# Optimization experiments

Hardware: AMD Instinct MI355X
Metric: run time of the kernel (lower is better)

The kernel has to match this reference:

```python
import jax, jax.numpy as jnp
import numpy as np

B, S, E, H = 8, 1024, 768, 12
D = E // H  # per-head dim


def setup_inputs() -> dict:
    key = jax.random.key(0)
    ks = jax.random.split(key, 9)
    glorot = lambda k: jax.random.normal(k, (E, E), jnp.float32) * np.sqrt(2.0 / (E + E))
    return {
        "inputs": jax.random.normal(ks[0], (B, S, E), jnp.float32),
        "Wq": glorot(ks[1]), "bq": jnp.zeros((E,), jnp.float32),
        "Wk": glorot(ks[2]), "bk": jnp.zeros((E,), jnp.float32),
        "Wv": glorot(ks[3]), "bv": jnp.zeros((E,), jnp.float32),
        "Wo": glorot(ks[4]), "bo": jnp.zeros((E,), jnp.float32),
    }


def reference(inputs, Wq, bq, Wk, bk, Wv, bv, Wo, bo):
    b, s, e = inputs.shape
    # QKV projections then split heads: [B,S,E] -> [B,H,S,D]
    def heads(x):
        return x.reshape(b, s, H, D).transpose(0, 2, 1, 3)
    q = heads(inputs @ Wq + bq)
    k = heads(inputs @ Wk + bk)
    v = heads(inputs @ Wv + bv)
    scale = 1.0 / jnp.sqrt(jnp.asarray(D, inputs.dtype))
    scores = jnp.einsum("bhqd,bhkd->bhqk", q, k) * scale
    weights = jax.nn.softmax(scores, axis=-1)  # attn_drop rate 0 -> identity
    attn = jnp.einsum("bhqk,bhkd->bhqd", weights, v)
    concat = attn.transpose(0, 2, 1, 3).reshape(b, s, e)
    out = concat @ Wo + bo  # proj_drop rate 0 -> identity
    return out
```

## Files before the change

### kernel.cpp

```cpp
#include <hip/hip_runtime.h>
#include <math.h>

#define BB 8
#define SS 1024
#define EE 768
#define HH 12
#define DD 64
#define MM (BB*SS)

typedef __attribute__((ext_vector_type(8))) short short8;
typedef __attribute__((ext_vector_type(4))) short short4v;
typedef __attribute__((ext_vector_type(4))) float f32x4;
typedef __attribute__((ext_vector_type(4))) int int4v;

static __device__ __forceinline__ short f2bf(float x) {
    unsigned u = __float_as_uint(x);
    u += 0x7fffu + ((u >> 16) & 1u);
    return (short)(u >> 16);
}
static __device__ __forceinline__ int cvtpk_bf16(float lo, float hi) {
    int r;
    asm("v_cvt_pk_bf16_f32 %0, %1, %2" : "=v"(r) : "v"(lo), "v"(hi));
    return r;
}
static __device__ __forceinline__ short8 i4_to_s8(int4v v) {
    union { int4v i; short8 s; } u; u.i = v; return u.s;
}

static __device__ __forceinline__ void gload_lds16(const void* g, void* l) {
    __builtin_amdgcn_global_load_lds((__attribute__((address_space(1))) void*)g,
                                     (__attribute__((address_space(3))) void*)l,
                                     16, 0, 0);
}

#define BAR __builtin_amdgcn_s_barrier()
#define VMW(n) asm volatile("s_waitcnt vmcnt(" #n ")" ::: "memory")

__global__ __launch_bounds__(256)
void prep(const float* __restrict__ X, short* __restrict__ Xb,
          const float* __restrict__ W0, const float* __restrict__ W1,
          const float* __restrict__ W2, const float* __restrict__ W3,
          short* __restrict__ Wt) {
    const int tid = threadIdx.x;
    if (blockIdx.x < 6144) {
        const long i = ((long)blockIdx.x * 256 + tid) * 4;
        float4 v = *(const float4*)&X[i];
        short4v o;
        o.x = f2bf(v.x); o.y = f2bf(v.y); o.z = f2bf(v.z); o.w = f2bf(v.w);
        *(short4v*)&Xb[i] = o;
        return;
    }
    __shared__ short T[64][72];
    const int id = blockIdx.x - 6144;
    const int z  = id / 144;
    const int r2 = id % 144;
    const int i0 = (r2 / 12) * 64;
    const int j0 = (r2 % 12) * 64;
    const float* sp = (z == 0) ? W0 : (z == 1) ? W1 : (z == 2) ? W2 : W3;
    short* dp = Wt + (long)z * EE * EE;
#pragma unroll
    for (int rep = 0; rep < 4; ++rep) {
        const int r = (tid >> 4) + rep * 16;
        const int c = (tid & 15) * 4;
        float4 v = *(const float4*)&sp[(long)(i0 + r) * EE + j0 + c];
        T[c + 0][r] = f2bf(v.x);
        T[c + 1][r] = f2bf(v.y);
        T[c + 2][r] = f2bf(v.z);
        T[c + 3][r] = f2bf(v.w);
    }
    __syncthreads();
#pragma unroll
    for (int rep = 0; rep < 4; ++rep) {
        const int rr = (tid >> 4) + rep * 16;
        const int cc = (tid & 15) * 4;
        short4v o;
        o.x = T[rr][cc + 0]; o.y = T[rr][cc + 1];
        o.z = T[rr][cc + 2]; o.w = T[rr][cc + 3];
        *(short4v*)&dp[(long)(j0 + rr) * EE + i0 + cc] = o;
    }
}

#define GEMM_CORE(Abase, Bbase, row0, col0)                                     \
    f32x4 acc[4][4];                                                            \
    _Pragma("unroll") for (int i = 0; i < 4; ++i)                               \
        _Pragma("unroll") for (int j = 0; j < 4; ++j)                           \
            acc[i][j] = (f32x4){0.f, 0.f, 0.f, 0.f};                            \
    const int rm = (w & 1) * 64, cn = (w >> 1) * 64;                            \
    for (int k0 = 0; k0 < EE; k0 += 64) {                                       \
        __syncthreads();                                                        \
        _Pragma("unroll") for (int i = 0; i < 4; ++i) {                         \
            const int chunk = w * 256 + i * 64 + lane;                          \
            const int r = chunk >> 3;                                          \
            const int cs = (((chunk & 7) ^ (r & 7)) << 3);                      \
            short* ldsA = Al + (w * 256 + i * 64) * 8;                          \
            short* ldsB = Bl + (w * 256 + i * 64) * 8;                          \
            gload_lds16(&Abase[(long)(row0 + r) * EE + k0 + cs], ldsA);         \
            gload_lds16(&Bbase[(long)(col0 + r) * EE + k0 + cs], ldsB);         \
        }                                                                       \
        __syncthreads();                                                        \
        _Pragma("unroll") for (int ks = 0; ks < 2; ++ks) {                      \
            short8 af[4], bf[4];                                                \
            _Pragma("unroll") for (int t = 0; t < 4; ++t)                       \
                af[t] = *(const short8*)&Al[(rm + t * 16 + m) * 64 +            \
                                            (((ks * 4 + quad) ^ (m & 7)) << 3)]; \
            _Pragma("unroll") for (int t = 0; t < 4; ++t)                       \
                bf[t] = *(const short8*)&Bl[(cn + t * 16 + m) * 64 +            \
                                            (((ks * 4 + quad) ^ (m & 7)) << 3)]; \
            _Pragma("unroll") for (int mt = 0; mt < 4; ++mt)                    \
                _Pragma("unroll") for (int nt = 0; nt < 4; ++nt)                \
                    acc[mt][nt] = __builtin_amdgcn_mfma_f32_16x16x32_bf16(      \
                        af[mt], bf[nt], acc[mt][nt], 0, 0, 0);                  \
        }                                                                       \
    }

#define QSCALE 0.1803368801111204f

#define STG1(Ld, Gbase, gr0, k0)                                              \
    do {                                                                      \
        const int r_ = tid >> 3;                                              \
        const int cs_ = ((tid & 7) ^ (r_ & 7)) << 3;                          \
        gload_lds16(&(Gbase)[(long)((gr0) + r_) * EE + (k0) + cs_],           \
                    (Ld) + w * 512);                                          \
    } while (0)

#define QKV_RDA(Ld, mb)                                                       \
    _Pragma("unroll") for (int t = 0; t < 4; ++t)                             \
        _Pragma("unroll") for (int ks = 0; ks < 2; ++ks)                      \
            af[t][ks] = *(const short8*)&(Ld)[(wr * 128 + ((mb) + t) * 16 + m) * 64 + \
                                              (((ks * 4 + quad) ^ (m & 7)) << 3)];

#define QKV_RDB(Ld)                                                           \
    _Pragma("unroll") for (int t = 0; t < 2; ++t)                             \
        _Pragma("unroll") for (int ks = 0; ks < 2; ++ks)                      \
            bf[t][ks] = *(const short8*)&(Ld)[(wc * 32 + t * 16 + m) * 64 +   \
                                              (((ks * 4 + quad) ^ (m & 7)) << 3)];

#define QKV_MF(mb)                                                            \
    __builtin_amdgcn_s_setprio(1);                                            \
    _Pragma("unroll") for (int mq = 0; mq < 4; ++mq)                          \
        _Pragma("unroll") for (int nq = 0; nq < 2; ++nq)                      \
            _Pragma("unroll") for (int ks = 0; ks < 2; ++ks)                  \
                acc[(mb) + mq][nq] = __builtin_amdgcn_mfma_f32_16x16x32_bf16( \
                    af[mq][ks], bf[nq][ks], acc[(mb) + mq][nq], 0, 0, 0);     \
    __builtin_amdgcn_s_setprio(0);

__global__ __launch_bounds__(512, 2)
void gemm_qkv(const short* __restrict__ Xb, const short* __restrict__ Wt,
              const float* __restrict__ bq, const float* __restrict__ bk,
              const float* __restrict__ bv,
              short* __restrict__ Qb, short* __restrict__ Kb,
              short* __restrict__ Vb) {
    __shared__ short SMEM[49152];
    short* const Ae = SMEM;
    short* const Ao = SMEM + 16384;
    short* const Be = SMEM + 32768;
    short* const Bo = SMEM + 40960;

    const int tid = threadIdx.x;
    const int w = tid >> 6;
    const int m = tid & 15, quad = (tid & 63) >> 4;
    const int wr = w >> 2, wc = w & 3;

    const int flat = blockIdx.x + 18 * blockIdx.y;
    const int id   = (flat & 7) * 72 + (flat >> 3);
    const int lcl  = id % 72;
    const int rt   = (id / 72) * 4 + (lcl & 3);
    const int ct   = lcl >> 2;
    const int row0 = rt * 256;
    const int wsel = ct / 6;
    const int col0w = (ct % 6) * 128;
    const short* Wsel = Wt + (long)wsel * EE * EE;
    const float* bias = (wsel == 0) ? bq : (wsel == 1) ? bk : bv;

    f32x4 acc[8][2];
#pragma unroll
    for (int i = 0; i < 8; ++i)
#pragma unroll
        for (int j = 0; j < 2; ++j) acc[i][j] = (f32x4){0.f, 0.f, 0.f, 0.f};

    STG1(Ae + 0,     Xb,   row0 + 0,    0);
    STG1(Ae + 8192,  Xb,   row0 + 128,  0);
    STG1(Be + 0,     Wsel, col0w + 0,   0);
    STG1(Be + 4096,  Wsel, col0w + 64,  0);
    STG1(Ae + 4096,  Xb,   row0 + 64,   0);
    STG1(Ae + 12288, Xb,   row0 + 192,  0);
    STG1(Bo + 0,     Wsel, col0w + 0,   64);
    STG1(Bo + 4096,  Wsel, col0w + 64,  64);
    STG1(Ao + 0,     Xb,   row0 + 0,    64);
    STG1(Ao + 8192,  Xb,   row0 + 128,  64);
    VMW(6);
    BAR;

#pragma unroll 1
    for (int it = 0; it < 6; ++it) {
        const int kO1 = (2 * it + 1) * 64;
        const int t2 = 2 * it + 2, t3 = 2 * it + 3;
        const int kE2 = (t2 < 12 ? t2 : 11) * 64;
        const int kO3 = (t3 < 12 ? t3 : 11) * 64;
        short8 af[4][2], bf[2][2];
        QKV_RDA(Ae, 0);
        QKV_RDB(Be);
        STG1(Ao + 4096,  Xb, row0 + 64,  kO1);
        STG1(Ao + 12288, Xb, row0 + 192, kO1);
        BAR;
        QKV_MF(0);
        VMW(6);
        BAR;
        QKV_RDA(Ae, 4);
        STG1(Be + 0,     Wsel, col0w + 0,  kE2);
        STG1(Be + 4096,  Wsel, col0w + 64, kE2);
        STG1(Ae + 0,     Xb,   row0 + 0,   kE2);
        STG1(Ae + 8192,  Xb,   row0 + 128, kE2);
        BAR;
        QKV_MF(4);
        VMW(6);
        BAR;
        QKV_RDA(Ao, 0);
        QKV_RDB(Bo);
        STG1(Ae + 4096,  Xb, row0 + 64,  kE2);
        STG1(Ae + 12288, Xb, row0 + 192, kE2);
        BAR;
        QKV_MF(0);
        VMW(6);
        BAR;
        QKV_RDA(Ao, 4);
        STG1(Bo + 0,     Wsel, col0w + 0,  kO3);
        STG1(Bo + 4096,  Wsel, col0w + 64, kO3);
        STG1(Ao + 0,     Xb,   row0 + 0,   kO3);
        STG1(Ao + 8192,  Xb,   row0 + 128, kO3);
        BAR;
        QKV_MF(4);
        VMW(6);
        BAR;
    }

    VMW(0);
    __syncthreads();
    const int b = row0 >> 10, s0 = row0 & 1023;
    short* EP = SMEM;

    if (wsel < 2) {
        const float scale = (wsel == 0) ? QSCALE : 1.0f;
        short* QK = (wsel == 0) ? Qb : Kb;
#pragma unroll
        for (int nt = 0; nt < 2; ++nt) {
            const float bvv = bias[col0w + wc * 32 + nt * 16 + m];
#pragma unroll
            for (int mt = 0; mt < 8; ++mt)
#pragma unroll
                for (int r = 0; r < 4; ++r)
                    EP[(wr * 128 + mt * 16 + quad * 4 + r) * 136 + wc * 32 + nt * 16 + m] =
                        f2bf((acc[mt][nt][r] + bvv) * scale);
        }
        __syncthreads();
#pragma unroll
        for (int rep = 0; rep < 8; ++rep) {
            const int chunk = tid + rep * 512;
            const int row = chunk >> 4;
            const int cc = (chunk & 15) * 8;
            const int colg = col0w + cc;
            const int h = colg >> 6, d = colg & 63;
            short8 v = *(const short8*)&EP[row * 136 + cc];
            *(short8*)&QK[((long)(b * HH + h) * SS + s0 + row) * DD + d] = v;
        }
    } else {
#pragma unroll
        for (int nt = 0; nt < 2; ++nt) {
            const float bvv = bias[col0w + wc * 32 + nt * 16 + m];
#pragma unroll
            for (int mt = 0; mt < 8; ++mt) {
                short4v o;
                o.x = f2bf(acc[mt][nt][0] + bvv);
                o.y = f2bf(acc[mt][nt][1] + bvv);
                o.z = f2bf(acc[mt][nt][2] + bvv);
                o.w = f2bf(acc[mt][nt][3] + bvv);
                *(short4v*)&EP[(wc * 32 + nt * 16 + m) * 264 + wr * 128 + mt * 16 + quad * 4] = o;
            }
        }
        __syncthreads();
#pragma unroll
        for (int rep = 0; rep < 8; ++rep) {
            const int chunk = tid + rep * 512;
            const int col = chunk >> 5;
            const int sc8 = (chunk & 31) * 8;
            const int colg = col0w + col;
            const int h = colg >> 6, d = colg & 63;
            short8 v = *(const short8*)&EP[col * 264 + sc8];
            *(short8*)&Vb[((long)(b * HH + h) * DD + d) * SS + s0 + sc8] = v;
        }
    }
}

__global__ __launch_bounds__(256)
void gemm_proj(const short* __restrict__ Cb, const short* __restrict__ WoT,
               const float* __restrict__ bo, float* __restrict__ out) {
    __shared__ short Al[128 * 64];
    __shared__ short Bl[128 * 64];
    const int tid = threadIdx.x, w = tid >> 6, lane = tid & 63;
    const int m = lane & 15, quad = lane >> 4;

    const int flat = blockIdx.x + 6 * blockIdx.y;
    const int id   = (flat & 7) * 48 + (flat >> 3);
    const int xcd  = id / 48;
    const int lcl  = id % 48;
    const int row0 = (xcd * 8 + (lcl & 7)) * 128;
    const int col0 = (lcl >> 3) * 128;

    GEMM_CORE(Cb, WoT, row0, col0)

#pragma unroll
    for (int nt = 0; nt < 4; ++nt) {
        const int colg = col0 + cn + nt * 16 + m;
        const float bvv = bo[colg];
#pragma unroll
        for (int mt = 0; mt < 4; ++mt)
#pragma unroll
            for (int r = 0; r < 4; ++r) {
                const int srow = row0 + rm + mt * 16 + quad * 4 + r;
                out[(long)srow * EE + colg] = acc[mt][nt][r] + bvv;
            }
    }
}

#define ATTN_STAGE(Kdst, Vdst, k0)                                            \
    do {                                                                      \
        _Pragma("unroll") for (int i = 0; i < 2; ++i) {                       \
            const int chunk = w * 128 + i * 64 + l;                           \
            const int r = chunk >> 3;                                         \
            const int cs = ((chunk & 7) ^ (r & 7)) << 3;                      \
            gload_lds16(&Kg[(long)((k0) + r) * DD + cs],                      \
                        (Kdst) + (w * 128 + i * 64) * 8);                     \
            gload_lds16(&Vg[(long)r * SS + (k0) + cs],                        \
                        (Vdst) + (w * 128 + i * 64) * 8);                     \
        }                                                                     \
    } while (0)

#define ATTN_COMPUTE(Kbuf, Vbuf)                                              \
    do {                                                                      \
        f32x4 sc[2][4];                                                       \
        __builtin_amdgcn_s_setprio(1);                                        \
        _Pragma("unroll") for (int nt = 0; nt < 4; ++nt) {                    \
            const short* kb = (Kbuf) + (nt * 16 + m) * 64;                    \
            short8 a0 = *(const short8*)&kb[(quad ^ (m & 7)) << 3];           \
            short8 a1 = *(const short8*)&kb[((4 + quad) ^ (m & 7)) << 3];     \
            _Pragma("unroll") for (int g = 0; g < 2; ++g) {                   \
                f32x4 a = (f32x4){0.f, 0.f, 0.f, 0.f};                        \
                a = __builtin_amdgcn_mfma_f32_16x16x32_bf16(a0, aq[g][0], a, 0, 0, 0); \
                a = __builtin_amdgcn_mfma_f32_16x16x32_bf16(a1, aq[g][1], a, 0, 0, 0); \
                sc[g][nt] = a;                                                \
            }                                                                 \
        }                                                                     \
        __builtin_amdgcn_s_setprio(0);                                        \
        _Pragma("unroll") for (int g = 0; g < 2; ++g)                         \
            _Pragma("unroll") for (int nt = 0; nt < 4; ++nt)                  \
                _Pragma("unroll") for (int r = 0; r < 4; ++r)                 \
                    sc[g][nt][r] = __builtin_amdgcn_exp2f(sc[g][nt][r]);      \
        short8 ap[2][2];                                                      \
        _Pragma("unroll") for (int g = 0; g < 2; ++g)                         \
            _Pragma("unroll") for (int hf = 0; hf < 2; ++hf) {                \
                int4v wv;                                                     \
                wv.x = cvtpk_bf16(sc[g][2 * hf + 0][0], sc[g][2 * hf + 0][1]); \
                wv.y = cvtpk_bf16(sc[g][2 * hf + 0][2], sc[g][2 * hf + 0][3]); \
                wv.z = cvtpk_bf16(sc[g][2 * hf + 1][0], sc[g][2 * hf + 1][1]); \
                wv.w = cvtpk_bf16(sc[g][2 * hf + 1][2], sc[g][2 * hf + 1][3]); \
                ap[g][hf] = i4_to_s8(wv);                                     \
            }                                                                 \
        __builtin_amdgcn_s_setprio(1);                                        \
        _Pragma("unroll") for (int g = 0; g < 2; ++g) {                       \
            lacc[g] = __builtin_amdgcn_mfma_f32_16x16x32_bf16(ap[g][0], ones, lacc[g], 0, 0, 0); \
            lacc[g] = __builtin_amdgcn_mfma_f32_16x16x32_bf16(ap[g][1], ones, lacc[g], 0, 0, 0); \
        }                                                                     \
        const int rsw = m & 7, hb = (quad & 1) * 4;                           \
        _Pragma("unroll") for (int dt = 0; dt < 4; ++dt) {                    \
            const short* vb = (Vbuf) + (dt * 16 + m) * 64;                    \
            short4v l0 = *(const short4v*)&vb[((((quad >> 1) + 0) ^ rsw) << 3) + hb]; \
            short4v h0 = *(const short4v*)&vb[((((quad >> 1) + 2) ^ rsw) << 3) + hb]; \
            short4v l1 = *(const short4v*)&vb[((((quad >> 1) + 4) ^ rsw) << 3) + hb]; \
            short4v h1 = *(const short4v*)&vb[((((quad >> 1) + 6) ^ rsw) << 3) + hb]; \
            short8 b0 = __builtin_shufflevector(l0, h0, 0, 1, 2, 3, 4, 5, 6, 7); \
            short8 b1 = __builtin_shufflevector(l1, h1, 0, 1, 2, 3, 4, 5, 6, 7); \
            _Pragma("unroll") for (int g = 0; g < 2; ++g) {                   \
                O[g][dt] = __builtin_amdgcn_mfma_f32_16x16x32_bf16(ap[g][0], b0, O[g][dt], 0, 0, 0); \
                O[g][dt] = __builtin_amdgcn_mfma_f32_16x16x32_bf16(ap[g][1], b1, O[g][dt], 0, 0, 0); \
            }                                                                 \
        }                                                                     \
        __builtin_amdgcn_s_setprio(0);                                        \
    } while (0)

__global__ __launch_bounds__(256)
void attn_mfma(const short* __restrict__ Q,
               const short* __restrict__ K,
               const short* __restrict__ Vt,
               short* __restrict__ out) {
    __shared__ short K0l[64 * 64];
    __shared__ short K1l[64 * 64];
    __shared__ short V0l[64 * 64];
    __shared__ short V1l[64 * 64];

    const int tid  = threadIdx.x;
    const int w    = tid >> 6;
    const int l    = tid & 63;
    const int m    = l & 15;
    const int quad = l >> 4;

    const int flat = blockIdx.x + 8 * blockIdx.y + 96 * blockIdx.z;
    const int id   = (flat & 7) * 96 + (flat >> 3);
    const int qt   = id & 7;
    const int bh   = id >> 3;
    const int b    = bh / HH;
    const int h    = bh % HH;
    const int q0   = qt * 128;

    const short* Qg = Q  + (long)bh * SS * DD;
    const short* Kg = K  + (long)bh * SS * DD;
    const short* Vg = Vt + (long)bh * DD * SS;

    short8 aq[2][2];
#pragma unroll
    for (int g = 0; g < 2; ++g) {
        const int row = q0 + w * 32 + g * 16 + m;
        aq[g][0] = *(const short8*)(Qg + (long)row * DD + quad * 8);
        aq[g][1] = *(const short8*)(Qg + (long)row * DD + 32 + quad * 8);
    }

    short8 ones;
#pragma unroll
    for (int i = 0; i < 8; ++i) ones[i] = (short)0x3F80;

    f32x4 O[2][4], lacc[2];
#pragma unroll
    for (int g = 0; g < 2; ++g) {
        lacc[g] = (f32x4){0.f, 0.f, 0.f, 0.f};
#pragma unroll
        for (int dt = 0; dt < 4; ++dt) O[g][dt] = (f32x4){0.f, 0.f, 0.f, 0.f};
    }

    ATTN_STAGE(K0l, V0l, 0);
    __syncthreads();

#pragma unroll 1
    for (int kt2 = 0; kt2 < 8; ++kt2) {
        const int k0 = kt2 * 128;
        ATTN_STAGE(K1l, V1l, k0 + 64);
        ATTN_COMPUTE(K0l, V0l);
        __syncthreads();
        if (kt2 < 7) ATTN_STAGE(K0l, V0l, k0 + 128);
        ATTN_COMPUTE(K1l, V1l);
        __syncthreads();
    }

#pragma unroll
    for (int g = 0; g < 2; ++g)
#pragma unroll
        for (int r = 0; r < 4; ++r) {
            const float inv = 1.0f / lacc[g][r];
            const int qo = q0 + w * 32 + g * 16 + quad * 4 + r;
            short* orow = out + ((long)(b * SS + qo)) * EE + h * DD;
#pragma unroll
            for (int dt = 0; dt < 4; ++dt)
                orow[dt * 16 + m] = f2bf(O[g][dt][r] * inv);
        }
}

extern "C" void kernel_launch(void* const* d_in, const int* in_sizes, int n_in,
                              void* d_out, int out_size, void* d_ws, size_t ws_size,
                              hipStream_t stream) {
    const float* X  = (const float*)d_in[0];
    const float* Wq = (const float*)d_in[1];
    const float* bq = (const float*)d_in[2];
    const float* Wk = (const float*)d_in[3];
    const float* bk = (const float*)d_in[4];
    const float* Wv = (const float*)d_in[5];
    const float* bv = (const float*)d_in[6];
    const float* Wo = (const float*)d_in[7];
    const float* bo = (const float*)d_in[8];

    const long SEG = (long)BB * HH * SS * DD;
    const long WSEG = (long)EE * EE;
    short* Xb = (short*)d_ws;
    short* Wt = Xb + SEG;
    short* Qb = Wt + 4 * WSEG;
    short* Kb = Qb + SEG;
    short* Vb = Kb + SEG;
    short* Cb = Vb + SEG;

    prep<<<dim3(6720), 256, 0, stream>>>(X, Xb, Wq, Wk, Wv, Wo, Wt);

    gemm_qkv<<<dim3(18, 32), 512, 0, stream>>>(Xb, Wt, bq, bk, bv, Qb, Kb, Vb);

    attn_mfma<<<dim3(SS / 128, HH, BB), 256, 0, stream>>>(Qb, Kb, Vb, Cb);

    gemm_proj<<<dim3(6, 64), 256, 0, stream>>>(Cb, Wt + 3 * WSEG, bo,
                                               (float*)d_out);
}
```

Baseline: 194.7 us.

## Reuse pipelined 256x128 QKV GEMM loop for output projection GEMM

Factors the double-buffered, software-pipelined 8-wave GEMM main loop from the QKV kernel into a shared macro and applies it to the output projection. The projection moves from 128x128 tiles with 256 threads and a single-buffered sync-heavy loop to 256x128 tiles with 512 threads, prefetching and overlapping loads with MFMA. The grid halves to 192 blocks, which may underfill the CUs on this GPU.

```diff
diff --git a/kernel.cpp b/kernel.cpp
--- a/kernel.cpp
+++ b/kernel.cpp
@@ -80,39 +80,6 @@
     }
 }
 
-#define GEMM_CORE(Abase, Bbase, row0, col0)                                     \
-    f32x4 acc[4][4];                                                            \
-    _Pragma("unroll") for (int i = 0; i < 4; ++i)                               \
-        _Pragma("unroll") for (int j = 0; j < 4; ++j)                           \
-            acc[i][j] = (f32x4){0.f, 0.f, 0.f, 0.f};                            \
-    const int rm = (w & 1) * 64, cn = (w >> 1) * 64;                            \
-    for (int k0 = 0; k0 < EE; k0 += 64) {                                       \
-        __syncthreads();                                                        \
-        _Pragma("unroll") for (int i = 0; i < 4; ++i) {                         \
-            const int chunk = w * 256 + i * 64 + lane;                          \
-            const int r = chunk >> 3;                                          \
-            const int cs = (((chunk & 7) ^ (r & 7)) << 3);                      \
-            short* ldsA = Al + (w * 256 + i * 64) * 8;                          \
-            short* ldsB = Bl + (w * 256 + i * 64) * 8;                          \
-            gload_lds16(&Abase[(long)(row0 + r) * EE + k0 + cs], ldsA);         \
-            gload_lds16(&Bbase[(long)(col0 + r) * EE + k0 + cs], ldsB);         \
-        }                                                                       \
-        __syncthreads();                                                        \
-        _Pragma("unroll") for (int ks = 0; ks < 2; ++ks) {                      \
-            short8 af[4], bf[4];                                                \
-            _Pragma("unroll") for (int t = 0; t < 4; ++t)                       \
-                af[t] = *(const short8*)&Al[(rm + t * 16 + m) * 64 +            \
-                                            (((ks * 4 + quad) ^ (m & 7)) << 3)]; \
-            _Pragma("unroll") for (int t = 0; t < 4; ++t)                       \
-                bf[t] = *(const short8*)&Bl[(cn + t * 16 + m) * 64 +            \
-                                            (((ks * 4 + quad) ^ (m & 7)) << 3)]; \
-            _Pragma("unroll") for (int mt = 0; mt < 4; ++mt)                    \
-                _Pragma("unroll") for (int nt = 0; nt < 4; ++nt)                \
-                    acc[mt][nt] = __builtin_amdgcn_mfma_f32_16x16x32_bf16(      \
-                        af[mt], bf[nt], acc[mt][nt], 0, 0, 0);                  \
-        }                                                                       \
-    }
-
 #define QSCALE 0.1803368801111204f
 
 #define STG1(Ld, Gbase, gr0, k0)                                              \
@@ -143,6 +110,62 @@
                 acc[(mb) + mq][nq] = __builtin_amdgcn_mfma_f32_16x16x32_bf16( \
                     af[mq][ks], bf[nq][ks], acc[(mb) + mq][nq], 0, 0, 0);     \
     __builtin_amdgcn_s_setprio(0);
+
+#define GEMM4P_LOOP(Abase, Bbase, row0, col0)                                 \
+    STG1(Ae + 0,     Abase, (row0) + 0,    0);                                \
+    STG1(Ae + 8192,  Abase, (row0) + 128,  0);                                \
+    STG1(Be + 0,     Bbase, (col0) + 0,    0);                                \
+    STG1(Be + 4096,  Bbase, (col0) + 64,   0);                                \
+    STG1(Ae + 4096,  Abase, (row0) + 64,   0);                                \
+    STG1(Ae + 12288, Abase, (row0) + 192,  0);                                \
+    STG1(Bo + 0,     Bbase, (col0) + 0,    64);                               \
+    STG1(Bo + 4096,  Bbase, (col0) + 64,   64);                               \
+    STG1(Ao + 0,     Abase, (row0) + 0,    64);                               \
+    STG1(Ao + 8192,  Abase, (row0) + 128,  64);                               \
+    VMW(6);                                                                   \
+    BAR;                                                                      \
+    _Pragma("unroll 1")                                                       \
+    for (int it = 0; it < 6; ++it) {                                          \
+        const int kO1 = (2 * it + 1) * 64;                                    \
+        const int t2 = 2 * it + 2, t3 = 2 * it + 3;                           \
+        const int kE2 = (t2 < 12 ? t2 : 11) * 64;                             \
+        const int kO3 = (t3 < 12 ? t3 : 11) * 64;                             \
+        short8 af[4][2], bf[2][2];                                            \
+        QKV_RDA(Ae, 0);                                                       \
+        QKV_RDB(Be);                                                          \
+        STG1(Ao + 4096,  Abase, (row0) + 64,  kO1);                           \
+        STG1(Ao + 12288, Abase, (row0) + 192, kO1);                           \
+        BAR;                                                                  \
+        QKV_MF(0);                                                            \
+        VMW(6);                                                               \
+        BAR;                                                                  \
+        QKV_RDA(Ae, 4);                                                       \
+        STG1(Be + 0,     Bbase, (col0) + 0,   kE2);                           \
+        STG1(Be + 4096,  Bbase, (col0) + 64,  kE2);                           \
+        STG1(Ae + 0,     Abase, (row0) + 0,   kE2);                           \
+        STG1(Ae + 8192,  Abase, (row0) + 128, kE2);                           \
+        BAR;                                                                  \
+        QKV_MF(4);                                                            \
+        VMW(6);                                                               \
+        BAR;                                                                  \
+        QKV_RDA(Ao, 0);                                                       \
+        QKV_RDB(Bo);                                                          \
+        STG1(Ae + 4096,  Abase, (row0) + 64,  kE2);                           \
+        STG1(Ae + 12288, Abase, (row0) + 192, kE2);                           \
+        BAR;                                                                  \
+        QKV_MF(0);                                                            \
+        VMW(6);                                                               \
+        BAR;                                                                  \
+        QKV_RDA(Ao, 4);                                                       \
+        STG1(Bo + 0,     Bbase, (col0) + 0,   kO3);                           \
+        STG1(Bo + 4096,  Bbase, (col0) + 64,  kO3);                           \
+        STG1(Ao + 0,     Abase, (row0) + 0,   kO3);                           \
+        STG1(Ao + 8192,  Abase, (row0) + 128, kO3);                           \
+        BAR;                                                                  \
+        QKV_MF(4);                                                            \
+        VMW(6);                                                               \
+        BAR;                                                                  \
+    }
 
 __global__ __launch_bounds__(512, 2)
 void gemm_qkv(const short* __restrict__ Xb, const short* __restrict__ Wt,
@@ -178,61 +201,7 @@
 #pragma unroll
         for (int j = 0; j < 2; ++j) acc[i][j] = (f32x4){0.f, 0.f, 0.f, 0.f};
 
-    STG1(Ae + 0,     Xb,   row0 + 0,    0);
-    STG1(Ae + 8192,  Xb,   row0 + 128,  0);
-    STG1(Be + 0,     Wsel, col0w + 0,   0);
-    STG1(Be + 4096,  Wsel, col0w + 64,  0);
-    STG1(Ae + 4096,  Xb,   row0 + 64,   0);
-    STG1(Ae + 12288, Xb,   row0 + 192,  0);
-    STG1(Bo + 0,     Wsel, col0w + 0,   64);
-    STG1(Bo + 4096,  Wsel, col0w + 64,  64);
-    STG1(Ao + 0,     Xb,   row0 + 0,    64);
-    STG1(Ao + 8192,  Xb,   row0 + 128,  64);
-    VMW(6);
-    BAR;
-
-#pragma unroll 1
-    for (int it = 0; it < 6; ++it) {
-        const int kO1 = (2 * it + 1) * 64;
-        const int t2 = 2 * it + 2, t3 = 2 * it + 3;
-        const int kE2 = (t2 < 12 ? t2 : 11) * 64;
-        const int kO3 = (t3 < 12 ? t3 : 11) * 64;
-        short8 af[4][2], bf[2][2];
-        QKV_RDA(Ae, 0);
-        QKV_RDB(Be);
-        STG1(Ao + 4096,  Xb, row0 + 64,  kO1);
-        STG1(Ao + 12288, Xb, row0 + 192, kO1);
-        BAR;
-        QKV_MF(0);
-        VMW(6);
-        BAR;
-        QKV_RDA(Ae, 4);
-        STG1(Be + 0,     Wsel, col0w + 0,  kE2);
-        STG1(Be + 4096,  Wsel, col0w + 64, kE2);
-        STG1(Ae + 0,     Xb,   row0 + 0,   kE2);
-        STG1(Ae + 8192,  Xb,   row0 + 128, kE2);
-        BAR;
-        QKV_MF(4);
-        VMW(6);
-        BAR;
-        QKV_RDA(Ao, 0);
-        QKV_RDB(Bo);
-        STG1(Ae + 4096,  Xb, row0 + 64,  kE2);
-        STG1(Ae + 12288, Xb, row0 + 192, kE2);
-        BAR;
-        QKV_MF(0);
-        VMW(6);
-        BAR;
-        QKV_RDA(Ao, 4);
-        STG1(Bo + 0,     Wsel, col0w + 0,  kO3);
-        STG1(Bo + 4096,  Wsel, col0w + 64, kO3);
-        STG1(Ao + 0,     Xb,   row0 + 0,   kO3);
-        STG1(Ao + 8192,  Xb,   row0 + 128, kO3);
-        BAR;
-        QKV_MF(4);
-        VMW(6);
-        BAR;
-    }
+    GEMM4P_LOOP(Xb, Wsel, row0, col0w)
 
     VMW(0);
     __syncthreads();
@@ -291,32 +260,47 @@
     }
 }
 
-__global__ __launch_bounds__(256)
+__global__ __launch_bounds__(512, 2)
 void gemm_proj(const short* __restrict__ Cb, const short* __restrict__ WoT,
                const float* __restrict__ bo, float* __restrict__ out) {
-    __shared__ short Al[128 * 64];
-    __shared__ short Bl[128 * 64];
-    const int tid = threadIdx.x, w = tid >> 6, lane = tid & 63;
-    const int m = lane & 15, quad = lane >> 4;
+    __shared__ short SMEM[49152];
+    short* const Ae = SMEM;
+    short* const Ao = SMEM + 16384;
+    short* const Be = SMEM + 32768;
+    short* const Bo = SMEM + 40960;
+
+    const int tid = threadIdx.x;
+    const int w = tid >> 6;
+    const int m = tid & 15, quad = (tid & 63) >> 4;
+    const int wr = w >> 2, wc = w & 3;
 
     const int flat = blockIdx.x + 6 * blockIdx.y;
-    const int id   = (flat & 7) * 48 + (flat >> 3);
-    const int xcd  = id / 48;
-    const int lcl  = id % 48;
-    const int row0 = (xcd * 8 + (lcl & 7)) * 128;
-    const int col0 = (lcl >> 3) * 128;
-
-    GEMM_CORE(Cb, WoT, row0, col0)
-
-#pragma unroll
-    for (int nt = 0; nt < 4; ++nt) {
-        const int colg = col0 + cn + nt * 16 + m;
+    const int id   = (flat & 7) * 24 + (flat >> 3);
+    const int lcl  = id % 24;
+    const int rt   = (id / 24) * 4 + (lcl & 3);
+    const int ct   = lcl >> 2;
+    const int row0 = rt * 256;
+    const int col0 = ct * 128;
+
+    f32x4 acc[8][2];
+#pragma unroll
+    for (int i = 0; i < 8; ++i)
+#pragma unroll
+        for (int j = 0; j < 2; ++j) acc[i][j] = (f32x4){0.f, 0.f, 0.f, 0.f};
+
+    GEMM4P_LOOP(Cb, WoT, row0, col0)
+
+    VMW(0);
+    __syncthreads();
+#pragma unroll
+    for (int nt = 0; nt < 2; ++nt) {
+        const int colg = col0 + wc * 32 + nt * 16 + m;
         const float bvv = bo[colg];
 #pragma unroll
-        for (int mt = 0; mt < 4; ++mt)
+        for (int mt = 0; mt < 8; ++mt)
 #pragma unroll
             for (int r = 0; r < 4; ++r) {
-                const int srow = row0 + rm + mt * 16 + quad * 4 + r;
+                const int srow = row0 + wr * 128 + mt * 16 + quad * 4 + r;
                 out[(long)srow * EE + colg] = acc[mt][nt][r] + bvv;
             }
     }
@@ -490,6 +474,6 @@
 
     attn_mfma<<<dim3(SS / 128, HH, BB), 256, 0, stream>>>(Qb, Kb, Vb, Cb);
 
-    gemm_proj<<<dim3(6, 64), 256, 0, stream>>>(Cb, Wt + 3 * WSEG, bo,
+    gemm_proj<<<dim3(6, 32), 512, 0, stream>>>(Cb, Wt + 3 * WSEG, bo,
                                                (float*)d_out);
 }
```

After: 192.4 us. No clear change (-1.2%).
